# Kernel optimization log

Measured on AMD Instinct MI355X. Metric: run time of the kernel, lower is better.

Reference implementation:

```python
import jax, jax.numpy as jnp
import numpy as np

N = 200_000   # nodes in batched graph
E = 400_000   # edges
D = 128       # embed_dim
L = 5         # num_layer
G = 1000      # number of graphs in batch
ATOM_V = 119  # atom vocab (OGB)
BOND_V = 5    # bond vocab (OGB)
OUT = 128     # output_dim
EPS = 1e-5


def setup_inputs() -> dict:
    key = jax.random.key(0)
    ks = jax.random.split(key, 16)
    inp = {
        "nfeat": jax.random.randint(ks[0], (N,), 0, ATOM_V),
        "efeat": jax.random.randint(ks[1], (E,), 0, BOND_V),
        "src": jax.random.randint(ks[2], (E,), 0, N),
        "dst": jax.random.randint(ks[3], (E,), 0, N),
        "node2graph": jnp.sort(jax.random.randint(ks[4], (N,), 0, G)),
        # learned parameters
        "atom_emb": jax.random.normal(ks[5], (ATOM_V, D), jnp.float32) * 0.02,
        "edge_emb": jax.random.normal(ks[6], (L, BOND_V, D), jnp.float32) * 0.02,
        "W": jax.random.normal(ks[7], (L, D, D), jnp.float32) * 0.02,
        "b": jnp.zeros((L, D), jnp.float32),
        "gamma": jnp.ones((L, D), jnp.float32),
        "beta": jnp.zeros((L, D), jnp.float32),
        "W1": jax.random.normal(ks[8], (D, D), jnp.float32) * 0.02,
        "b1": jnp.zeros((D,), jnp.float32),
        "W2": jax.random.normal(ks[9], (D, OUT), jnp.float32) * 0.02,
        "b2": jnp.zeros((OUT,), jnp.float32),
    }
    return inp


def reference(nfeat, efeat, src, dst, node2graph,
              atom_emb, edge_emb, W, b, gamma, beta, W1, b1, W2, b2):
    h = atom_emb[nfeat]                                  # [N, D]
    # in-degree + 1 (GCNConvLayer degree norm)
    deg = jax.ops.segment_sum(jnp.ones((E,), h.dtype), dst, num_segments=N) + 1.0
    for l in range(L):
        e = edge_emb[l][efeat]                           # [E, D] edge encoder
        m = h[src] + e                                   # u_add_e
        neigh = jax.ops.segment_sum(m, dst, num_segments=N)  # fn.sum -> 'neigh'
        h = ((h + neigh) / deg[:, None]) @ W[l] + b[l]   # project_node_feat
        # batch norm over nodes (training-mode batch stats), affine
        mu = jnp.mean(h, axis=0)
        var = jnp.var(h, axis=0)
        h = (h - mu) * jax.lax.rsqrt(var + EPS) * gamma[l] + beta[l]
        h = jax.nn.relu(h)                               # activation; dropout=eval
    # global mean pooling per graph
    cnt = jax.ops.segment_sum(jnp.ones((N,), h.dtype), node2graph, num_segments=G)
    g = jax.ops.segment_sum(h, node2graph, num_segments=G) / jnp.maximum(cnt, 1.0)[:, None]
    # predict MLP (dropout in eval mode = identity)
    out = jax.nn.relu(g @ W1 + b1) @ W2 + b2             # [G, OUT]
    return out
```

## Files before the change

### kernel.cpp

```cpp
#include <hip/hip_runtime.h>
#include <hip/hip_bf16.h>
#include <cstddef>

#define NN 200000
#define NE 400000
#define DD 128
#define NL 5
#define NG 1000
#define BOND_V 5
#define BM 32
#define NBLK (NN / BM)
#define CAPE 256
#define CHUNK 200
#define NB_SCAN 200
#define CH 1000
#define EPS 1e-5f
#define XS 136

typedef __bf16 bf16x8 __attribute__((ext_vector_type(8)));
typedef float floatx4 __attribute__((ext_vector_type(4)));

__device__ __forceinline__ unsigned short f2bf(float f) {
    unsigned int u = __float_as_uint(f);
    u = (u + 0x7fffu + ((u >> 16) & 1u)) >> 16;
    return (unsigned short)u;
}
__device__ __forceinline__ float bf2f(unsigned short s) {
    return __uint_as_float(((unsigned int)s) << 16);
}

__global__ void k_deg_int(const int* __restrict__ dst, int* __restrict__ cnt) {
    int e = blockIdx.x * blockDim.x + threadIdx.x;
    if (e < NE) atomicAdd(&cnt[dst[e]], 1);
}

__global__ void k_cnt(const int* __restrict__ n2g, float* __restrict__ gcnt) {
    int n = blockIdx.x * blockDim.x + threadIdx.x;
    if (n < NN) atomicAdd(&gcnt[n2g[n]], 1.0f);
}

__global__ void k_rdeg(const int* __restrict__ cnt, float* __restrict__ rdeg) {
    int n = blockIdx.x * blockDim.x + threadIdx.x;
    if (n < NN) rdeg[n] = 1.0f / (float)(cnt[n] + 1);
}

__global__ void k_scan1(const int* __restrict__ cnt, int* __restrict__ bsum) {
    __shared__ int sh[256];
    int b = blockIdx.x, t = threadIdx.x;
    int s = 0;
    if (t < CH / 4) {
        int base = b * CH + t * 4;
        s = cnt[base] + cnt[base + 1] + cnt[base + 2] + cnt[base + 3];
    }
    sh[t] = s;
    __syncthreads();
    if (t == 0) {
        int tot = 0;
        for (int i = 0; i < CH / 4; i++) tot += sh[i];
        bsum[b] = tot;
    }
}

__global__ void k_scan2(const int* __restrict__ bsum, int* __restrict__ bpre,
                        int* __restrict__ off) {
    if (threadIdx.x == 0) {
        int run = 0;
        for (int i = 0; i < NB_SCAN; i++) { bpre[i] = run; run += bsum[i]; }
        off[NN] = NE;
    }
}

__global__ void k_scan3(const int* __restrict__ cnt, const int* __restrict__ bpre,
                        int* __restrict__ off, int* __restrict__ cur) {
    __shared__ int sh[256];
    int b = blockIdx.x, t = threadIdx.x;
    int base = b * CH + t * 4;
    int c0 = 0, c1 = 0, c2 = 0, c3 = 0, s = 0;
    if (t < CH / 4) {
        c0 = cnt[base]; c1 = cnt[base + 1]; c2 = cnt[base + 2]; c3 = cnt[base + 3];
        s = c0 + c1 + c2 + c3;
    }
    sh[t] = s;
    __syncthreads();
    if (t == 0) {
        int run = bpre[b];
        for (int i = 0; i < CH / 4; i++) { int v = sh[i]; sh[i] = run; run += v; }
    }
    __syncthreads();
    if (t < CH / 4) {
        int run = sh[t];
        off[base] = run; cur[base] = run; run += c0;
        off[base + 1] = run; cur[base + 1] = run; run += c1;
        off[base + 2] = run; cur[base + 2] = run; run += c2;
        off[base + 3] = run; cur[base + 3] = run;
    }
}

__global__ void k_bucket(const int* __restrict__ src, const int* __restrict__ dst,
                         const int* __restrict__ efeat, int* __restrict__ cur,
                         int* __restrict__ esrc, int* __restrict__ eft) {
    int e = blockIdx.x * blockDim.x + threadIdx.x;
    if (e < NE) {
        int p = atomicAdd(&cur[dst[e]], 1);
        esrc[p] = src[e];
        eft[p] = efeat[e];
    }
}

__global__ void k_wsplit(const float* __restrict__ W, unsigned short* __restrict__ Wht,
                         unsigned short* __restrict__ Wlt) {
    int idx = blockIdx.x * 256 + threadIdx.x;
    if (idx >= NL * DD * DD) return;
    int l = idx / (DD * DD), rem = idx % (DD * DD);
    int k = rem / DD, n = rem % DD;
    float v = W[idx];
    unsigned short hb = f2bf(v);
    unsigned short lb = f2bf(v - bf2f(hb));
    size_t o = (size_t)l * DD * DD + (size_t)n * DD + k;
    Wht[o] = hb; Wlt[o] = lb;
}

__device__ __forceinline__ float4 bnrelu4(float4 x, float4 m, float4 r, float4 g, float4 b) {
    float4 o;
    o.x = fmaxf(0.f, (x.x - m.x) * r.x * g.x + b.x);
    o.y = fmaxf(0.f, (x.y - m.y) * r.y * g.y + b.y);
    o.z = fmaxf(0.f, (x.z - m.z) * r.z * g.z + b.z);
    o.w = fmaxf(0.f, (x.w - m.w) * r.w * g.w + b.w);
    return o;
}

__global__ __launch_bounds__(256)
void k_fused(const float* __restrict__ base, const int* __restrict__ nfeat, int first,
             const int* __restrict__ off, const int* __restrict__ esrc,
             const int* __restrict__ eft, const float* __restrict__ eemb,
             const float* __restrict__ rdeg,
             const float* __restrict__ mu, const float* __restrict__ rsig,
             const float* __restrict__ gamma, const float* __restrict__ beta,
             const unsigned short* __restrict__ Wht, const unsigned short* __restrict__ Wlt,
             const float* __restrict__ bias,
             float* __restrict__ C, float* __restrict__ part) {
    __shared__ unsigned short Xh[BM * XS];
    __shared__ unsigned short Xl[BM * XS];
    __shared__ float eS[BOND_V * DD];
    __shared__ float red[4 * DD];
    __shared__ int esL[CAPE], efL[CAPE];
    __shared__ int offL[BM + 1];

    int tid = threadIdx.x;
    int n0 = blockIdx.x * BM;
    if (tid < BOND_V * DD / 4)
        *(float4*)(eS + tid * 4) = *(const float4*)(eemb + tid * 4);
    if (tid <= BM) offL[tid] = off[n0 + tid];
    int e_beg = off[n0], e_end = off[n0 + BM];
    for (int e = e_beg + tid; e < e_end; e += 256) {
        int idx = e - e_beg;
        if (idx < CAPE) { esL[idx] = esrc[e]; efL[idx] = eft[e]; }
    }

    int lane32 = tid & 31, grp = tid >> 5;
    int c4 = lane32 << 2;
    float4 m4, r4, g4, b4;
    if (!first) {
        m4 = *(const float4*)(mu + c4);
        r4 = *(const float4*)(rsig + c4);
        g4 = *(const float4*)(gamma + c4);
        b4 = *(const float4*)(beta + c4);
    }
    __syncthreads();

    bool lds_ok = (e_end - e_beg) <= CAPE;

    for (int i = 0; i < 4; i++) {
        int r = grp * 4 + i;
        int n = n0 + r;
        int rown = first ? nfeat[n] : n;
        float4 acc = *(const float4*)(base + (size_t)rown * DD + c4);
        if (!first) acc = bnrelu4(acc, m4, r4, g4, b4);
        int e0 = offL[r], e1 = offL[r + 1];
        int k = e0;
        if (lds_ok) {
            for (; k + 1 < e1; k += 2) {
                int i0 = k - e_beg;
                int s0 = esL[i0], f0 = efL[i0];
                int s1 = esL[i0 + 1], f1 = efL[i0 + 1];
                if (first) { s0 = nfeat[s0]; s1 = nfeat[s1]; }
                float4 h0 = *(const float4*)(base + (size_t)s0 * DD + c4);
                float4 h1 = *(const float4*)(base + (size_t)s1 * DD + c4);
                if (!first) { h0 = bnrelu4(h0, m4, r4, g4, b4); h1 = bnrelu4(h1, m4, r4, g4, b4); }
                float4 ev0 = *(const float4*)(eS + f0 * DD + c4);
                float4 ev1 = *(const float4*)(eS + f1 * DD + c4);
                acc.x += h0.x + ev0.x + h1.x + ev1.x;
                acc.y += h0.y + ev0.y + h1.y + ev1.y;
                acc.z += h0.z + ev0.z + h1.z + ev1.z;
                acc.w += h0.w + ev0.w + h1.w + ev1.w;
            }
            if (k < e1) {
                int i0 = k - e_beg;
                int s0 = esL[i0], f0 = efL[i0];
                if (first) s0 = nfeat[s0];
                float4 h0 = *(const float4*)(base + (size_t)s0 * DD + c4);
                if (!first) h0 = bnrelu4(h0, m4, r4, g4, b4);
                float4 ev0 = *(const float4*)(eS + f0 * DD + c4);
                acc.x += h0.x + ev0.x; acc.y += h0.y + ev0.y;
                acc.z += h0.z + ev0.z; acc.w += h0.w + ev0.w;
            }
        } else {
            for (; k < e1; k++) {
                int s0 = esrc[k], f0 = eft[k];
                if (first) s0 = nfeat[s0];
                float4 h0 = *(const float4*)(base + (size_t)s0 * DD + c4);
                if (!first) h0 = bnrelu4(h0, m4, r4, g4, b4);
                float4 ev0 = *(const float4*)(eS + f0 * DD + c4);
                acc.x += h0.x + ev0.x; acc.y += h0.y + ev0.y;
                acc.z += h0.z + ev0.z; acc.w += h0.w + ev0.w;
            }
        }
        float rd = rdeg[n];
        acc.x *= rd; acc.y *= rd; acc.z *= rd; acc.w *= rd;
        unsigned short h0 = f2bf(acc.x), h1 = f2bf(acc.y), h2 = f2bf(acc.z), h3 = f2bf(acc.w);
        unsigned short l0 = f2bf(acc.x - bf2f(h0));
        unsigned short l1 = f2bf(acc.y - bf2f(h1));
        unsigned short l2 = f2bf(acc.z - bf2f(h2));
        unsigned short l3 = f2bf(acc.w - bf2f(h3));
        uint2 hv2, lv2;
        hv2.x = (unsigned)h0 | ((unsigned)h1 << 16);
        hv2.y = (unsigned)h2 | ((unsigned)h3 << 16);
        lv2.x = (unsigned)l0 | ((unsigned)l1 << 16);
        lv2.y = (unsigned)l2 | ((unsigned)l3 << 16);
        *(uint2*)(Xh + r * XS + c4) = hv2;
        *(uint2*)(Xl + r * XS + c4) = lv2;
    }
    __syncthreads();

    int lane = tid & 63, w = tid >> 6;
    int m16 = lane & 15, quad = lane >> 4;
    int rowTile = w & 1;
    int colBase = (w >> 1) << 6;
    int rowA = rowTile * 16 + m16;

    floatx4 acc4[4];
    #pragma unroll
    for (int t = 0; t < 4; t++) acc4[t] = (floatx4){0.f, 0.f, 0.f, 0.f};

    #pragma unroll
    for (int kp = 0; kp < 4; kp++) {
        bf16x8 ah = *(const bf16x8*)(Xh + rowA * XS + kp * 32 + quad * 8);
        bf16x8 al = *(const bf16x8*)(Xl + rowA * XS + kp * 32 + quad * 8);
        #pragma unroll
        for (int t = 0; t < 4; t++) {
            int ncol = colBase + t * 16 + m16;
            bf16x8 bh = *(const bf16x8*)(Wht + (size_t)ncol * DD + kp * 32 + quad * 8);
            bf16x8 bl = *(const bf16x8*)(Wlt + (size_t)ncol * DD + kp * 32 + quad * 8);
            acc4[t] = __builtin_amdgcn_mfma_f32_16x16x32_bf16(ah, bh, acc4[t], 0, 0, 0);
            acc4[t] = __builtin_amdgcn_mfma_f32_16x16x32_bf16(ah, bl, acc4[t], 0, 0, 0);
            acc4[t] = __builtin_amdgcn_mfma_f32_16x16x32_bf16(al, bh, acc4[t], 0, 0, 0);
        }
    }

    float* redS = red;
    float* redQ = red + 2 * DD;
    #pragma unroll
    for (int t = 0; t < 4; t++) {
        int col = colBase + t * 16 + m16;
        float bv = bias[col];
        float s = 0.f, q = 0.f;
        #pragma unroll
        for (int rr = 0; rr < 4; rr++) {
            float v = acc4[t][rr] + bv;
            C[(size_t)(n0 + rowTile * 16 + quad * 4 + rr) * DD + col] = v;
            s += v; q += v * v;
        }
        s += __shfl_xor(s, 16); q += __shfl_xor(q, 16);
        s += __shfl_xor(s, 32); q += __shfl_xor(q, 32);
        if (lane < 16) { redS[rowTile * DD + col] = s; redQ[rowTile * DD + col] = q; }
    }
    __syncthreads();
    if (tid < DD) {
        float ss = redS[tid] + redS[DD + tid];
        float qq = redQ[tid] + redQ[DD + tid];
        part[(size_t)tid * NBLK + blockIdx.x] = ss;
        part[(size_t)(DD + tid) * NBLK + blockIdx.x] = qq;
    }
}

__global__ void k_stats(const float* __restrict__ part,
                        float* __restrict__ mu, float* __restrict__ rsig) {
    int col = blockIdx.x;
    float s = 0.f, q = 0.f;
    for (int i = threadIdx.x; i < NBLK; i += 256) {
        s += part[(size_t)col * NBLK + i];
        q += part[(size_t)(DD + col) * NBLK + i];
    }
    #pragma unroll
    for (int o = 32; o > 0; o >>= 1) {
        s += __shfl_down(s, o);
        q += __shfl_down(q, o);
    }
    __shared__ float sh[8];
    int lane = threadIdx.x & 63, w = threadIdx.x >> 6;
    if (lane == 0) { sh[w] = s; sh[4 + w] = q; }
    __syncthreads();
    if (threadIdx.x == 0) {
        float S = sh[0] + sh[1] + sh[2] + sh[3];
        float Q = sh[4] + sh[5] + sh[6] + sh[7];
        float m = S / (float)NN;
        float v = Q / (float)NN - m * m;
        mu[col] = m;
        rsig[col] = rsqrtf(v + EPS);
    }
}

__global__ void k_bnpool(const float* __restrict__ A, const int* __restrict__ n2g,
                         const float* __restrict__ mu, const float* __restrict__ rsig,
                         const float* __restrict__ gamma, const float* __restrict__ beta,
                         float* __restrict__ gsum) {
    int j = threadIdx.x;
    int n0 = blockIdx.x * CHUNK;
    float m = mu[j], r = rsig[j], ga = gamma[j], be = beta[j];
    int cur = n2g[n0];
    float acc = 0.f;
    for (int i = 0; i < CHUNK; i++) {
        int n = n0 + i;
        int gg = n2g[n];
        if (gg != cur) {
            atomicAdd(&gsum[(size_t)cur * DD + j], acc);
            acc = 0.f;
            cur = gg;
        }
        float x = A[(size_t)n * DD + j];
        x = fmaxf(0.f, (x - m) * r * ga + be);
        acc += x;
    }
    atomicAdd(&gsum[(size_t)cur * DD + j], acc);
}

__global__ void k_mlp(const float* __restrict__ gsum, const float* __restrict__ gcnt,
                      const float* __restrict__ W1, const float* __restrict__ b1,
                      const float* __restrict__ W2, const float* __restrict__ b2,
                      float* __restrict__ out) {
    __shared__ float gs[DD], hs[DD];
    int gid = blockIdx.x, j = threadIdx.x;
    float inv = 1.0f / fmaxf(gcnt[gid], 1.0f);
    gs[j] = gsum[(size_t)gid * DD + j] * inv;
    __syncthreads();
    float a = b1[j];
    for (int k = 0; k < DD; k++) a += gs[k] * W1[k * DD + j];
    hs[j] = fmaxf(a, 0.f);
    __syncthreads();
    float o = b2[j];
    for (int k = 0; k < DD; k++) o += hs[k] * W2[k * DD + j];
    out[(size_t)gid * DD + j] = o;
}

extern "C" void kernel_launch(void* const* d_in, const int* in_sizes, int n_in,
                              void* d_out, int out_size, void* d_ws, size_t ws_size,
                              hipStream_t stream) {
    const int*   nfeat = (const int*)d_in[0];
    const int*   efeat = (const int*)d_in[1];
    const int*   src   = (const int*)d_in[2];
    const int*   dst   = (const int*)d_in[3];
    const int*   n2g   = (const int*)d_in[4];
    const float* aemb  = (const float*)d_in[5];
    const float* eemb  = (const float*)d_in[6];
    const float* Wl    = (const float*)d_in[7];
    const float* bl    = (const float*)d_in[8];
    const float* gam   = (const float*)d_in[9];
    const float* bet   = (const float*)d_in[10];
    const float* W1    = (const float*)d_in[11];
    const float* b1    = (const float*)d_in[12];
    const float* W2    = (const float*)d_in[13];
    const float* b2    = (const float*)d_in[14];
    float* out = (float*)d_out;

    float* ws   = (float*)d_ws;
    float* H0   = ws;
    float* H1   = H0 + (size_t)NN * DD;
    float* rdeg = H1 + (size_t)NN * DD;
    float* gsum = rdeg + NN;
    float* gcnt = gsum + (size_t)NG * DD;
    float* mu   = gcnt + NG;
    float* rsg  = mu + DD;
    float* part = rsg + DD;
    unsigned short* Wht = (unsigned short*)(part + (size_t)2 * DD * NBLK);
    unsigned short* Wlt = Wht + (size_t)NL * DD * DD;
    int* off  = (int*)(Wlt + (size_t)NL * DD * DD);
    int* cur  = off + NN + 1;
    int* esrc = cur + NN;
    int* eft  = esrc + NE;
    int* cnt  = (int*)part;
    int* bsum = (int*)part + 300000;
    int* bpre = (int*)part + 301000;

    hipMemsetAsync(cnt, 0, (size_t)NN * sizeof(int), stream);
    hipMemsetAsync(gsum, 0, (size_t)(NG * DD + NG) * sizeof(float), stream);

    k_deg_int<<<(NE + 255) / 256, 256, 0, stream>>>(dst, cnt);
    k_cnt<<<(NN + 255) / 256, 256, 0, stream>>>(n2g, gcnt);
    k_scan1<<<NB_SCAN, 256, 0, stream>>>(cnt, bsum);
    k_scan2<<<1, 64, 0, stream>>>(bsum, bpre, off);
    k_scan3<<<NB_SCAN, 256, 0, stream>>>(cnt, bpre, off, cur);
    k_rdeg<<<(NN + 255) / 256, 256, 0, stream>>>(cnt, rdeg);
    k_bucket<<<(NE + 255) / 256, 256, 0, stream>>>(src, dst, efeat, cur, esrc, eft);
    k_wsplit<<<(NL * DD * DD + 255) / 256, 256, 0, stream>>>(Wl, Wht, Wlt);

    float* hcur = H0;
    for (int l = 0; l < NL; l++) {
        const float* base = (l == 0) ? aemb : hcur;
        float* hnext = (l == 0) ? H0 : ((hcur == H0) ? H1 : H0);
        const float* g_prev = (l == 0) ? gam : gam + (size_t)(l - 1) * DD;
        const float* b_prev = (l == 0) ? bet : bet + (size_t)(l - 1) * DD;
        k_fused<<<NBLK, 256, 0, stream>>>(base, nfeat, (l == 0) ? 1 : 0,
                                          off, esrc, eft,
                                          eemb + (size_t)l * BOND_V * DD, rdeg,
                                          mu, rsg, g_prev, b_prev,
                                          Wht + (size_t)l * DD * DD,
                                          Wlt + (size_t)l * DD * DD,
                                          bl + (size_t)l * DD, hnext, part);
        k_stats<<<DD, 256, 0, stream>>>(part, mu, rsg);
        hcur = hnext;
    }
    k_bnpool<<<NN / CHUNK, DD, 0, stream>>>(hcur, n2g, mu, rsg,
                                            gam + (size_t)(NL - 1) * DD,
                                            bet + (size_t)(NL - 1) * DD, gsum);
    k_mlp<<<NG, DD, 0, stream>>>(gsum, gcnt, W1, b1, W2, b2, out);
}
```

Before: 1.143 ms.

## Fuse setup kernels, edge-parallel LDS atomics, and last-block BN stats reduction

Merges the degree count, graph count and weight split into one setup kernel, and folds the reciprocal-degree computation into the scan. The per-node edge loop in the fused layer kernel becomes an edge-parallel loop. It accumulates into an fp32 LDS tile with shared-memory atomics, using the destination row packed into the edge feature word. The separate BN stats kernel is replaced by sharded global atomics with a last-block-done reduction inside the fused kernel. This removes launches and load imbalance between nodes of different degree, at the cost of LDS atomic contention and extra syncs.

```diff
diff --git a/kernel.cpp b/kernel.cpp
--- a/kernel.cpp
+++ b/kernel.cpp
@@ -16,6 +16,8 @@
 #define CH 1000
 #define EPS 1e-5f
 #define XS 136
+#define XFS 132
+#define NSH 32
 
 typedef __bf16 bf16x8 __attribute__((ext_vector_type(8)));
 typedef float floatx4 __attribute__((ext_vector_type(4)));
@@ -29,19 +31,22 @@
     return __uint_as_float(((unsigned int)s) << 16);
 }
 
-__global__ void k_deg_int(const int* __restrict__ dst, int* __restrict__ cnt) {
+__global__ void k_setup1(const int* __restrict__ dst, int* __restrict__ cnt,
+                         const int* __restrict__ n2g, float* __restrict__ gcnt,
+                         const float* __restrict__ W, unsigned short* __restrict__ Wht,
+                         unsigned short* __restrict__ Wlt) {
     int e = blockIdx.x * blockDim.x + threadIdx.x;
     if (e < NE) atomicAdd(&cnt[dst[e]], 1);
-}
-
-__global__ void k_cnt(const int* __restrict__ n2g, float* __restrict__ gcnt) {
-    int n = blockIdx.x * blockDim.x + threadIdx.x;
-    if (n < NN) atomicAdd(&gcnt[n2g[n]], 1.0f);
-}
-
-__global__ void k_rdeg(const int* __restrict__ cnt, float* __restrict__ rdeg) {
-    int n = blockIdx.x * blockDim.x + threadIdx.x;
-    if (n < NN) rdeg[n] = 1.0f / (float)(cnt[n] + 1);
+    if (e < NN) atomicAdd(&gcnt[n2g[e]], 1.0f);
+    if (e < NL * DD * DD) {
+        int l = e / (DD * DD), rem = e % (DD * DD);
+        int k = rem / DD, n = rem % DD;
+        float v = W[e];
+        unsigned short hb = f2bf(v);
+        unsigned short lb = f2bf(v - bf2f(hb));
+        size_t o = (size_t)l * DD * DD + (size_t)n * DD + k;
+        Wht[o] = hb; Wlt[o] = lb;
+    }
 }
 
 __global__ void k_scan1(const int* __restrict__ cnt, int* __restrict__ bsum) {
@@ -71,7 +76,8 @@
 }
 
 __global__ void k_scan3(const int* __restrict__ cnt, const int* __restrict__ bpre,
-                        int* __restrict__ off, int* __restrict__ cur) {
+                        int* __restrict__ off, int* __restrict__ cur,
+                        float* __restrict__ rdeg) {
     __shared__ int sh[256];
     int b = blockIdx.x, t = threadIdx.x;
     int base = b * CH + t * 4;
@@ -93,31 +99,23 @@
         off[base + 1] = run; cur[base + 1] = run; run += c1;
         off[base + 2] = run; cur[base + 2] = run; run += c2;
         off[base + 3] = run; cur[base + 3] = run;
+        rdeg[base]     = 1.0f / (float)(c0 + 1);
+        rdeg[base + 1] = 1.0f / (float)(c1 + 1);
+        rdeg[base + 2] = 1.0f / (float)(c2 + 1);
+        rdeg[base + 3] = 1.0f / (float)(c3 + 1);
     }
 }
 
 __global__ void k_bucket(const int* __restrict__ src, const int* __restrict__ dst,
                          const int* __restrict__ efeat, int* __restrict__ cur,
-                         int* __restrict__ esrc, int* __restrict__ eft) {
+                         int* __restrict__ esrc, int* __restrict__ epk) {
     int e = blockIdx.x * blockDim.x + threadIdx.x;
     if (e < NE) {
-        int p = atomicAdd(&cur[dst[e]], 1);
+        int d = dst[e];
+        int p = atomicAdd(&cur[d], 1);
         esrc[p] = src[e];
-        eft[p] = efeat[e];
-    }
-}
-
-__global__ void k_wsplit(const float* __restrict__ W, unsigned short* __restrict__ Wht,
-                         unsigned short* __restrict__ Wlt) {
-    int idx = blockIdx.x * 256 + threadIdx.x;
-    if (idx >= NL * DD * DD) return;
-    int l = idx / (DD * DD), rem = idx % (DD * DD);
-    int k = rem / DD, n = rem % DD;
-    float v = W[idx];
-    unsigned short hb = f2bf(v);
-    unsigned short lb = f2bf(v - bf2f(hb));
-    size_t o = (size_t)l * DD * DD + (size_t)n * DD + k;
-    Wht[o] = hb; Wlt[o] = lb;
+        epk[p] = efeat[e] | ((d & (BM - 1)) << 8);
+    }
 }
 
 __device__ __forceinline__ float4 bnrelu4(float4 x, float4 m, float4 r, float4 g, float4 b) {
@@ -132,96 +130,103 @@
 __global__ __launch_bounds__(256)
 void k_fused(const float* __restrict__ base, const int* __restrict__ nfeat, int first,
              const int* __restrict__ off, const int* __restrict__ esrc,
-             const int* __restrict__ eft, const float* __restrict__ eemb,
+             const int* __restrict__ epk, const float* __restrict__ eemb,
              const float* __restrict__ rdeg,
-             const float* __restrict__ mu, const float* __restrict__ rsig,
+             const float* __restrict__ muP, const float* __restrict__ rsP,
              const float* __restrict__ gamma, const float* __restrict__ beta,
              const unsigned short* __restrict__ Wht, const unsigned short* __restrict__ Wlt,
              const float* __restrict__ bias,
-             float* __restrict__ C, float* __restrict__ part) {
-    __shared__ unsigned short Xh[BM * XS];
-    __shared__ unsigned short Xl[BM * XS];
+             float* __restrict__ C,
+             float* __restrict__ musum, float* __restrict__ varsum,
+             int* __restrict__ cntL, float* __restrict__ muO, float* __restrict__ rsO) {
+    __shared__ float4 uni4[1088];
+    float* Xf = (float*)uni4;
+    unsigned short* Xh = (unsigned short*)uni4;
+    unsigned short* Xl = Xh + 4352;
     __shared__ float eS[BOND_V * DD];
     __shared__ float red[4 * DD];
-    __shared__ int esL[CAPE], efL[CAPE];
-    __shared__ int offL[BM + 1];
+    __shared__ int esL[CAPE], epkL[CAPE];
+    __shared__ int lastFlag;
 
     int tid = threadIdx.x;
     int n0 = blockIdx.x * BM;
     if (tid < BOND_V * DD / 4)
         *(float4*)(eS + tid * 4) = *(const float4*)(eemb + tid * 4);
-    if (tid <= BM) offL[tid] = off[n0 + tid];
     int e_beg = off[n0], e_end = off[n0 + BM];
+    int nE = e_end - e_beg;
     for (int e = e_beg + tid; e < e_end; e += 256) {
         int idx = e - e_beg;
-        if (idx < CAPE) { esL[idx] = esrc[e]; efL[idx] = eft[e]; }
+        if (idx < CAPE) { esL[idx] = esrc[e]; epkL[idx] = epk[e]; }
     }
 
     int lane32 = tid & 31, grp = tid >> 5;
     int c4 = lane32 << 2;
     float4 m4, r4, g4, b4;
     if (!first) {
-        m4 = *(const float4*)(mu + c4);
-        r4 = *(const float4*)(rsig + c4);
+        m4 = *(const float4*)(muP + c4);
+        r4 = *(const float4*)(rsP + c4);
         g4 = *(const float4*)(gamma + c4);
         b4 = *(const float4*)(beta + c4);
     }
-    __syncthreads();
-
-    bool lds_ok = (e_end - e_beg) <= CAPE;
-
+
+    #pragma unroll
     for (int i = 0; i < 4; i++) {
         int r = grp * 4 + i;
         int n = n0 + r;
         int rown = first ? nfeat[n] : n;
         float4 acc = *(const float4*)(base + (size_t)rown * DD + c4);
         if (!first) acc = bnrelu4(acc, m4, r4, g4, b4);
-        int e0 = offL[r], e1 = offL[r + 1];
-        int k = e0;
-        if (lds_ok) {
-            for (; k + 1 < e1; k += 2) {
-                int i0 = k - e_beg;
-                int s0 = esL[i0], f0 = efL[i0];
-                int s1 = esL[i0 + 1], f1 = efL[i0 + 1];
-                if (first) { s0 = nfeat[s0]; s1 = nfeat[s1]; }
-                float4 h0 = *(const float4*)(base + (size_t)s0 * DD + c4);
-                float4 h1 = *(const float4*)(base + (size_t)s1 * DD + c4);
-                if (!first) { h0 = bnrelu4(h0, m4, r4, g4, b4); h1 = bnrelu4(h1, m4, r4, g4, b4); }
-                float4 ev0 = *(const float4*)(eS + f0 * DD + c4);
-                float4 ev1 = *(const float4*)(eS + f1 * DD + c4);
-                acc.x += h0.x + ev0.x + h1.x + ev1.x;
-                acc.y += h0.y + ev0.y + h1.y + ev1.y;
-                acc.z += h0.z + ev0.z + h1.z + ev1.z;
-                acc.w += h0.w + ev0.w + h1.w + ev1.w;
-            }
-            if (k < e1) {
-                int i0 = k - e_beg;
-                int s0 = esL[i0], f0 = efL[i0];
-                if (first) s0 = nfeat[s0];
-                float4 h0 = *(const float4*)(base + (size_t)s0 * DD + c4);
-                if (!first) h0 = bnrelu4(h0, m4, r4, g4, b4);
-                float4 ev0 = *(const float4*)(eS + f0 * DD + c4);
-                acc.x += h0.x + ev0.x; acc.y += h0.y + ev0.y;
-                acc.z += h0.z + ev0.z; acc.w += h0.w + ev0.w;
-            }
-        } else {
-            for (; k < e1; k++) {
-                int s0 = esrc[k], f0 = eft[k];
-                if (first) s0 = nfeat[s0];
-                float4 h0 = *(const float4*)(base + (size_t)s0 * DD + c4);
-                if (!first) h0 = bnrelu4(h0, m4, r4, g4, b4);
-                float4 ev0 = *(const float4*)(eS + f0 * DD + c4);
-                acc.x += h0.x + ev0.x; acc.y += h0.y + ev0.y;
-                acc.z += h0.z + ev0.z; acc.w += h0.w + ev0.w;
-            }
-        }
-        float rd = rdeg[n];
-        acc.x *= rd; acc.y *= rd; acc.z *= rd; acc.w *= rd;
-        unsigned short h0 = f2bf(acc.x), h1 = f2bf(acc.y), h2 = f2bf(acc.z), h3 = f2bf(acc.w);
-        unsigned short l0 = f2bf(acc.x - bf2f(h0));
-        unsigned short l1 = f2bf(acc.y - bf2f(h1));
-        unsigned short l2 = f2bf(acc.z - bf2f(h2));
-        unsigned short l3 = f2bf(acc.w - bf2f(h3));
+        *(float4*)(Xf + r * XFS + c4) = acc;
+    }
+    __syncthreads();
+
+    if (nE <= CAPE) {
+        for (int k = grp; k < nE; k += 8) {
+            int s = esL[k], pk = epkL[k];
+            if (first) s = nfeat[s];
+            float4 hv = *(const float4*)(base + (size_t)s * DD + c4);
+            if (!first) hv = bnrelu4(hv, m4, r4, g4, b4);
+            const float* ep = eS + (pk & 255) * DD + c4;
+            float* xp = Xf + (pk >> 8) * XFS + c4;
+            atomicAdd(xp + 0, hv.x + ep[0]);
+            atomicAdd(xp + 1, hv.y + ep[1]);
+            atomicAdd(xp + 2, hv.z + ep[2]);
+            atomicAdd(xp + 3, hv.w + ep[3]);
+        }
+    } else {
+        for (int k = e_beg + grp; k < e_end; k += 8) {
+            int s = esrc[k], pk = epk[k];
+            if (first) s = nfeat[s];
+            float4 hv = *(const float4*)(base + (size_t)s * DD + c4);
+            if (!first) hv = bnrelu4(hv, m4, r4, g4, b4);
+            const float* ep = eS + (pk & 255) * DD + c4;
+            float* xp = Xf + (pk >> 8) * XFS + c4;
+            atomicAdd(xp + 0, hv.x + ep[0]);
+            atomicAdd(xp + 1, hv.y + ep[1]);
+            atomicAdd(xp + 2, hv.z + ep[2]);
+            atomicAdd(xp + 3, hv.w + ep[3]);
+        }
+    }
+    __syncthreads();
+
+    float4 v[4];
+    #pragma unroll
+    for (int i = 0; i < 4; i++) {
+        int r = grp * 4 + i;
+        v[i] = *(const float4*)(Xf + r * XFS + c4);
+        float rd = rdeg[n0 + r];
+        v[i].x *= rd; v[i].y *= rd; v[i].z *= rd; v[i].w *= rd;
+    }
+    __syncthreads();
+
+    #pragma unroll
+    for (int i = 0; i < 4; i++) {
+        int r = grp * 4 + i;
+        unsigned short h0 = f2bf(v[i].x), h1 = f2bf(v[i].y), h2 = f2bf(v[i].z), h3 = f2bf(v[i].w);
+        unsigned short l0 = f2bf(v[i].x - bf2f(h0));
+        unsigned short l1 = f2bf(v[i].y - bf2f(h1));
+        unsigned short l2 = f2bf(v[i].z - bf2f(h2));
+        unsigned short l3 = f2bf(v[i].w - bf2f(h3));
         uint2 hv2, lv2;
         hv2.x = (unsigned)h0 | ((unsigned)h1 << 16);
         hv2.y = (unsigned)h2 | ((unsigned)h3 << 16);
@@ -266,47 +271,37 @@
         float s = 0.f, q = 0.f;
         #pragma unroll
         for (int rr = 0; rr < 4; rr++) {
-            float v = acc4[t][rr] + bv;
-            C[(size_t)(n0 + rowTile * 16 + quad * 4 + rr) * DD + col] = v;
-            s += v; q += v * v;
+            float vv = acc4[t][rr] + bv;
+            C[(size_t)(n0 + rowTile * 16 + quad * 4 + rr) * DD + col] = vv;
+            s += vv; q += vv * vv;
         }
         s += __shfl_xor(s, 16); q += __shfl_xor(q, 16);
         s += __shfl_xor(s, 32); q += __shfl_xor(q, 32);
         if (lane < 16) { redS[rowTile * DD + col] = s; redQ[rowTile * DD + col] = q; }
     }
     __syncthreads();
+    int shard = blockIdx.x & (NSH - 1);
     if (tid < DD) {
         float ss = redS[tid] + redS[DD + tid];
         float qq = redQ[tid] + redQ[DD + tid];
-        part[(size_t)tid * NBLK + blockIdx.x] = ss;
-        part[(size_t)(DD + tid) * NBLK + blockIdx.x] = qq;
-    }
-}
-
-__global__ void k_stats(const float* __restrict__ part,
-                        float* __restrict__ mu, float* __restrict__ rsig) {
-    int col = blockIdx.x;
-    float s = 0.f, q = 0.f;
-    for (int i = threadIdx.x; i < NBLK; i += 256) {
-        s += part[(size_t)col * NBLK + i];
-        q += part[(size_t)(DD + col) * NBLK + i];
-    }
-    #pragma unroll
-    for (int o = 32; o > 0; o >>= 1) {
-        s += __shfl_down(s, o);
-        q += __shfl_down(q, o);
-    }
-    __shared__ float sh[8];
-    int lane = threadIdx.x & 63, w = threadIdx.x >> 6;
-    if (lane == 0) { sh[w] = s; sh[4 + w] = q; }
-    __syncthreads();
-    if (threadIdx.x == 0) {
-        float S = sh[0] + sh[1] + sh[2] + sh[3];
-        float Q = sh[4] + sh[5] + sh[6] + sh[7];
+        atomicAdd(&musum[tid * NSH + shard], ss);
+        atomicAdd(&varsum[tid * NSH + shard], qq);
+        __threadfence();
+    }
+    __syncthreads();
+    if (tid == 0) lastFlag = (atomicAdd(cntL, 1) == NBLK - 1);
+    __syncthreads();
+    if (lastFlag && tid < DD) {
+        float S = 0.f, Q = 0.f;
+        #pragma unroll
+        for (int sh = 0; sh < NSH; sh++) {
+            S += atomicAdd(&musum[tid * NSH + sh], 0.0f);
+            Q += atomicAdd(&varsum[tid * NSH + sh], 0.0f);
+        }
         float m = S / (float)NN;
-        float v = Q / (float)NN - m * m;
-        mu[col] = m;
-        rsig[col] = rsqrtf(v + EPS);
+        float va = Q / (float)NN - m * m;
+        muO[tid] = m;
+        rsO[tid] = rsqrtf(va + EPS);
     }
 }
 
@@ -372,54 +367,62 @@
     const float* b2    = (const float*)d_in[14];
     float* out = (float*)d_out;
 
-    float* ws   = (float*)d_ws;
-    float* H0   = ws;
-    float* H1   = H0 + (size_t)NN * DD;
-    float* rdeg = H1 + (size_t)NN * DD;
-    float* gsum = rdeg + NN;
-    float* gcnt = gsum + (size_t)NG * DD;
-    float* mu   = gcnt + NG;
-    float* rsg  = mu + DD;
-    float* part = rsg + DD;
-    unsigned short* Wht = (unsigned short*)(part + (size_t)2 * DD * NBLK);
+    float* ws    = (float*)d_ws;
+    float* H0    = ws;
+    float* H1    = H0 + (size_t)NN * DD;
+    float* rdeg  = H1 + (size_t)NN * DD;
+    float* gsum  = rdeg + NN;
+    float* gcnt  = gsum + (size_t)NG * DD;
+    float* muA   = gcnt + NG;
+    float* rsA   = muA + NL * DD;
+    float* musum = rsA + NL * DD;
+    float* varsum= musum + (size_t)NL * DD * NSH;
+    int*   cntL  = (int*)(varsum + (size_t)NL * DD * NSH);
+    unsigned short* Wht = (unsigned short*)(cntL + 16);
     unsigned short* Wlt = Wht + (size_t)NL * DD * DD;
     int* off  = (int*)(Wlt + (size_t)NL * DD * DD);
     int* cur  = off + NN + 1;
     int* esrc = cur + NN;
-    int* eft  = esrc + NE;
-    int* cnt  = (int*)part;
-    int* bsum = (int*)part + 300000;
-    int* bpre = (int*)part + 301000;
-
+    int* epk  = esrc + NE;
+    int* cnt  = epk + NE;
+    int* bsum = cnt + NN;
+    int* bpre = bsum + NB_SCAN;
+
+    hipMemsetAsync(gsum, 0, (size_t)(NG * DD + NG) * sizeof(float), stream);
+    hipMemsetAsync(musum, 0, (size_t)(2 * NL * DD * NSH) * sizeof(float) + 16 * sizeof(int), stream);
     hipMemsetAsync(cnt, 0, (size_t)NN * sizeof(int), stream);
-    hipMemsetAsync(gsum, 0, (size_t)(NG * DD + NG) * sizeof(float), stream);
-
-    k_deg_int<<<(NE + 255) / 256, 256, 0, stream>>>(dst, cnt);
-    k_cnt<<<(NN + 255) / 256, 256, 0, stream>>>(n2g, gcnt);
+
+    k_setup1<<<(NE + 255) / 256, 256, 0, stream>>>(dst, cnt, n2g, gcnt, Wl, Wht, Wlt);
     k_scan1<<<NB_SCAN, 256, 0, stream>>>(cnt, bsum);
     k_scan2<<<1, 64, 0, stream>>>(bsum, bpre, off);
-    k_scan3<<<NB_SCAN, 256, 0, stream>>>(cnt, bpre, off, cur);
-    k_rdeg<<<(NN + 255) / 256, 256, 0, stream>>>(cnt, rdeg);
-    k_bucket<<<(NE + 255) / 256, 256, 0, stream>>>(src, dst, efeat, cur, esrc, eft);
-    k_wsplit<<<(NL * DD * DD + 255) / 256, 256, 0, stream>>>(Wl, Wht, Wlt);
+    k_scan3<<<NB_SCAN, 256, 0, stream>>>(cnt, bpre, off, cur, rdeg);
+    k_bucket<<<(NE + 255) / 256, 256, 0, stream>>>(src, dst, efeat, cur, esrc, epk);
 
     float* hcur = H0;
     for (int l = 0; l < NL; l++) {
         const float* base = (l == 0) ? aemb : hcur;
         float* hnext = (l == 0) ? H0 : ((hcur == H0) ? H1 : H0);
+        const float* muP = (l == 0) ? muA : muA + (size_t)(l - 1) * DD;
+        const float* rsP = (l == 0) ? rsA : rsA + (size_t)(l - 1) * DD;
         const float* g_prev = (l == 0) ? gam : gam + (size_t)(l - 1) * DD;
         const float* b_prev = (l == 0) ? bet : bet + (size_t)(l - 1) * DD;
         k_fused<<<NBLK, 256, 0, stream>>>(base, nfeat, (l == 0) ? 1 : 0,
-                                          off, esrc, eft,
+                                          off, esrc, epk,
                                           eemb + (size_t)l * BOND_V * DD, rdeg,
-                                          mu, rsg, g_prev, b_prev,
+                                          muP, rsP, g_prev, b_prev,
                                           Wht + (size_t)l * DD * DD,
                                           Wlt + (size_t)l * DD * DD,
-                                          bl + (size_t)l * DD, hnext, part);
-        k_stats<<<DD, 256, 0, stream>>>(part, mu, rsg);
+                                          bl + (size_t)l * DD, hnext,
+                                          musum + (size_t)l * DD * NSH,
+                                          varsum + (size_t)l * DD * NSH,
+                                          cntL + l,
+                                          muA + (size_t)l * DD,
+                                          rsA + (size_t)l * DD);
         hcur = hnext;
     }
-    k_bnpool<<<NN / CHUNK, DD, 0, stream>>>(hcur, n2g, mu, rsg,
+    k_bnpool<<<NN / CHUNK, DD, 0, stream>>>(hcur, n2g,
+                                            muA + (size_t)(NL - 1) * DD,
+                                            rsA + (size_t)(NL - 1) * DD,
                                             gam + (size_t)(NL - 1) * DD,
                                             bet + (size_t)(NL - 1) * DD, gsum);
     k_mlp<<<NG, DD, 0, stream>>>(gsum, gcnt, W1, b1, W2, b2, out);
```

Measured after the change: 3.401 ms. +197.5%, slower.

## Pad per-block edge lists into column-major packed layout for batched gathers

Applied to the files above, without the earlier changes.

Adds a preprocessing kernel that, for each 32-node block, packs each node's first 16 incoming edges (source index plus bond type in one int) into a padded column-major array, with a dummy bond type that maps to a zero row. The aggregation loop then processes four rows per step with independent gathers, which is meant to raise memory-level parallelism and remove the per-block LDS staging and its sync. Edges beyond 16 fall back to a scalar loop. Setup kernels are also merged (degree count, graph count and weight split in one launch; reciprocal degree folded into the scan), which trims launch overhead. The cost is wasted loads on padded slots when degrees within a block differ.

```diff
diff --git a/kernel.cpp b/kernel.cpp
--- a/kernel.cpp
+++ b/kernel.cpp
@@ -10,7 +10,7 @@
 #define BOND_V 5
 #define BM 32
 #define NBLK (NN / BM)
-#define CAPE 256
+#define MAXD 16
 #define CHUNK 200
 #define NB_SCAN 200
 #define CH 1000
@@ -29,19 +29,22 @@
     return __uint_as_float(((unsigned int)s) << 16);
 }
 
-__global__ void k_deg_int(const int* __restrict__ dst, int* __restrict__ cnt) {
+__global__ void k_setup1(const int* __restrict__ dst, int* __restrict__ cnt,
+                         const int* __restrict__ n2g, float* __restrict__ gcnt,
+                         const float* __restrict__ W, unsigned short* __restrict__ Wht,
+                         unsigned short* __restrict__ Wlt) {
     int e = blockIdx.x * blockDim.x + threadIdx.x;
     if (e < NE) atomicAdd(&cnt[dst[e]], 1);
-}
-
-__global__ void k_cnt(const int* __restrict__ n2g, float* __restrict__ gcnt) {
-    int n = blockIdx.x * blockDim.x + threadIdx.x;
-    if (n < NN) atomicAdd(&gcnt[n2g[n]], 1.0f);
-}
-
-__global__ void k_rdeg(const int* __restrict__ cnt, float* __restrict__ rdeg) {
-    int n = blockIdx.x * blockDim.x + threadIdx.x;
-    if (n < NN) rdeg[n] = 1.0f / (float)(cnt[n] + 1);
+    if (e < NN) atomicAdd(&gcnt[n2g[e]], 1.0f);
+    if (e < NL * DD * DD) {
+        int l = e / (DD * DD), rem = e % (DD * DD);
+        int k = rem / DD, n = rem % DD;
+        float v = W[e];
+        unsigned short hb = f2bf(v);
+        unsigned short lb = f2bf(v - bf2f(hb));
+        size_t o = (size_t)l * DD * DD + (size_t)n * DD + k;
+        Wht[o] = hb; Wlt[o] = lb;
+    }
 }
 
 __global__ void k_scan1(const int* __restrict__ cnt, int* __restrict__ bsum) {
@@ -71,7 +74,8 @@
 }
 
 __global__ void k_scan3(const int* __restrict__ cnt, const int* __restrict__ bpre,
-                        int* __restrict__ off, int* __restrict__ cur) {
+                        int* __restrict__ off, int* __restrict__ cur,
+                        float* __restrict__ rdeg) {
     __shared__ int sh[256];
     int b = blockIdx.x, t = threadIdx.x;
     int base = b * CH + t * 4;
@@ -93,6 +97,10 @@
         off[base + 1] = run; cur[base + 1] = run; run += c1;
         off[base + 2] = run; cur[base + 2] = run; run += c2;
         off[base + 3] = run; cur[base + 3] = run;
+        rdeg[base]     = 1.0f / (float)(c0 + 1);
+        rdeg[base + 1] = 1.0f / (float)(c1 + 1);
+        rdeg[base + 2] = 1.0f / (float)(c2 + 1);
+        rdeg[base + 3] = 1.0f / (float)(c3 + 1);
     }
 }
 
@@ -107,17 +115,30 @@
     }
 }
 
-__global__ void k_wsplit(const float* __restrict__ W, unsigned short* __restrict__ Wht,
-                         unsigned short* __restrict__ Wlt) {
-    int idx = blockIdx.x * 256 + threadIdx.x;
-    if (idx >= NL * DD * DD) return;
-    int l = idx / (DD * DD), rem = idx % (DD * DD);
-    int k = rem / DD, n = rem % DD;
-    float v = W[idx];
-    unsigned short hb = f2bf(v);
-    unsigned short lb = f2bf(v - bf2f(hb));
-    size_t o = (size_t)l * DD * DD + (size_t)n * DD + k;
-    Wht[o] = hb; Wlt[o] = lb;
+__global__ void k_pad(const int* __restrict__ off, const int* __restrict__ esrc,
+                      const int* __restrict__ eft, int* __restrict__ pent,
+                      int* __restrict__ bmaxd) {
+    __shared__ int offL[BM + 1];
+    __shared__ int mx;
+    int b = blockIdx.x, tid = threadIdx.x;
+    if (tid == 0) mx = 0;
+    if (tid <= BM) offL[tid] = off[b * BM + tid];
+    __syncthreads();
+    if (tid < BM) atomicMax(&mx, offL[tid + 1] - offL[tid]);
+    __syncthreads();
+    int maxd = mx;
+    if (tid == 0) bmaxd[b] = maxd;
+    int jmax = maxd < MAXD ? maxd : MAXD;
+    int tot = jmax * BM;
+    int* pb = pent + (size_t)b * MAXD * BM;
+    for (int idx = tid; idx < tot; idx += 256) {
+        int j = idx >> 5, r = idx & 31;
+        int d = offL[r + 1] - offL[r];
+        int v;
+        if (j < d) { int e = offL[r] + j; v = esrc[e] | (eft[e] << 18); }
+        else v = (5 << 18);
+        pb[idx] = v;
+    }
 }
 
 __device__ __forceinline__ float4 bnrelu4(float4 x, float4 m, float4 r, float4 g, float4 b) {
@@ -132,96 +153,114 @@
 __global__ __launch_bounds__(256)
 void k_fused(const float* __restrict__ base, const int* __restrict__ nfeat, int first,
              const int* __restrict__ off, const int* __restrict__ esrc,
-             const int* __restrict__ eft, const float* __restrict__ eemb,
+             const int* __restrict__ eft, const int* __restrict__ pent,
+             const int* __restrict__ bmaxd, const float* __restrict__ eemb,
              const float* __restrict__ rdeg,
-             const float* __restrict__ mu, const float* __restrict__ rsig,
+             const float* __restrict__ muP, const float* __restrict__ rsP,
              const float* __restrict__ gamma, const float* __restrict__ beta,
              const unsigned short* __restrict__ Wht, const unsigned short* __restrict__ Wlt,
              const float* __restrict__ bias,
              float* __restrict__ C, float* __restrict__ part) {
     __shared__ unsigned short Xh[BM * XS];
     __shared__ unsigned short Xl[BM * XS];
-    __shared__ float eS[BOND_V * DD];
+    __shared__ float eS[6 * DD];
     __shared__ float red[4 * DD];
-    __shared__ int esL[CAPE], efL[CAPE];
     __shared__ int offL[BM + 1];
 
     int tid = threadIdx.x;
     int n0 = blockIdx.x * BM;
-    if (tid < BOND_V * DD / 4)
-        *(float4*)(eS + tid * 4) = *(const float4*)(eemb + tid * 4);
+    if (tid < 160) *(float4*)(eS + tid * 4) = *(const float4*)(eemb + tid * 4);
+    else if (tid < 192) *(float4*)(eS + tid * 4) = (float4){0.f, 0.f, 0.f, 0.f};
     if (tid <= BM) offL[tid] = off[n0 + tid];
-    int e_beg = off[n0], e_end = off[n0 + BM];
-    for (int e = e_beg + tid; e < e_end; e += 256) {
-        int idx = e - e_beg;
-        if (idx < CAPE) { esL[idx] = esrc[e]; efL[idx] = eft[e]; }
-    }
 
     int lane32 = tid & 31, grp = tid >> 5;
     int c4 = lane32 << 2;
     float4 m4, r4, g4, b4;
     if (!first) {
-        m4 = *(const float4*)(mu + c4);
-        r4 = *(const float4*)(rsig + c4);
+        m4 = *(const float4*)(muP + c4);
+        r4 = *(const float4*)(rsP + c4);
         g4 = *(const float4*)(gamma + c4);
         b4 = *(const float4*)(beta + c4);
     }
     __syncthreads();
 
-    bool lds_ok = (e_end - e_beg) <= CAPE;
-
+    float4 acc[4];
+    #pragma unroll
+    for (int i = 0; i < 4; i++) {
+        int n = n0 + grp * 4 + i;
+        int rown = first ? nfeat[n] : n;
+        float4 a = *(const float4*)(base + (size_t)rown * DD + c4);
+        if (!first) a = bnrelu4(a, m4, r4, g4, b4);
+        acc[i] = a;
+    }
+
+    int maxd = bmaxd[blockIdx.x];
+    int jmax = maxd < MAXD ? maxd : MAXD;
+    const int* pb = pent + (size_t)blockIdx.x * MAXD * BM + grp * 4;
+    for (int j = 0; j < jmax; j++) {
+        int v0 = pb[j * BM + 0];
+        int v1 = pb[j * BM + 1];
+        int v2 = pb[j * BM + 2];
+        int v3 = pb[j * BM + 3];
+        int s0 = v0 & 0x3FFFF, f0 = v0 >> 18;
+        int s1 = v1 & 0x3FFFF, f1 = v1 >> 18;
+        int s2 = v2 & 0x3FFFF, f2 = v2 >> 18;
+        int s3 = v3 & 0x3FFFF, f3 = v3 >> 18;
+        if (first) { s0 = nfeat[s0]; s1 = nfeat[s1]; s2 = nfeat[s2]; s3 = nfeat[s3]; }
+        float4 h0 = *(const float4*)(base + (size_t)s0 * DD + c4);
+        float4 h1 = *(const float4*)(base + (size_t)s1 * DD + c4);
+        float4 h2 = *(const float4*)(base + (size_t)s2 * DD + c4);
+        float4 h3 = *(const float4*)(base + (size_t)s3 * DD + c4);
+        if (!first) {
+            h0 = bnrelu4(h0, m4, r4, g4, b4);
+            h1 = bnrelu4(h1, m4, r4, g4, b4);
+            h2 = bnrelu4(h2, m4, r4, g4, b4);
+            h3 = bnrelu4(h3, m4, r4, g4, b4);
+        }
+        float w0 = (f0 == 5) ? 0.f : 1.f;
+        float w1 = (f1 == 5) ? 0.f : 1.f;
+        float w2 = (f2 == 5) ? 0.f : 1.f;
+        float w3 = (f3 == 5) ? 0.f : 1.f;
+        float4 e0 = *(const float4*)(eS + f0 * DD + c4);
+        float4 e1 = *(const float4*)(eS + f1 * DD + c4);
+        float4 e2 = *(const float4*)(eS + f2 * DD + c4);
+        float4 e3 = *(const float4*)(eS + f3 * DD + c4);
+        acc[0].x += (h0.x + e0.x) * w0; acc[0].y += (h0.y + e0.y) * w0;
+        acc[0].z += (h0.z + e0.z) * w0; acc[0].w += (h0.w + e0.w) * w0;
+        acc[1].x += (h1.x + e1.x) * w1; acc[1].y += (h1.y + e1.y) * w1;
+        acc[1].z += (h1.z + e1.z) * w1; acc[1].w += (h1.w + e1.w) * w1;
+        acc[2].x += (h2.x + e2.x) * w2; acc[2].y += (h2.y + e2.y) * w2;
+        acc[2].z += (h2.z + e2.z) * w2; acc[2].w += (h2.w + e2.w) * w2;
+        acc[3].x += (h3.x + e3.x) * w3; acc[3].y += (h3.y + e3.y) * w3;
+        acc[3].z += (h3.z + e3.z) * w3; acc[3].w += (h3.w + e3.w) * w3;
+    }
+
+    if (maxd > MAXD) {
+        #pragma unroll
+        for (int i = 0; i < 4; i++) {
+            int r = grp * 4 + i;
+            for (int e = offL[r] + MAXD; e < offL[r + 1]; e++) {
+                int s = esrc[e], f = eft[e];
+                if (first) s = nfeat[s];
+                float4 hv = *(const float4*)(base + (size_t)s * DD + c4);
+                if (!first) hv = bnrelu4(hv, m4, r4, g4, b4);
+                const float* ep = eS + f * DD + c4;
+                acc[i].x += hv.x + ep[0]; acc[i].y += hv.y + ep[1];
+                acc[i].z += hv.z + ep[2]; acc[i].w += hv.w + ep[3];
+            }
+        }
+    }
+
+    #pragma unroll
     for (int i = 0; i < 4; i++) {
         int r = grp * 4 + i;
-        int n = n0 + r;
-        int rown = first ? nfeat[n] : n;
-        float4 acc = *(const float4*)(base + (size_t)rown * DD + c4);
-        if (!first) acc = bnrelu4(acc, m4, r4, g4, b4);
-        int e0 = offL[r], e1 = offL[r + 1];
-        int k = e0;
-        if (lds_ok) {
-            for (; k + 1 < e1; k += 2) {
-                int i0 = k - e_beg;
-                int s0 = esL[i0], f0 = efL[i0];
-                int s1 = esL[i0 + 1], f1 = efL[i0 + 1];
-                if (first) { s0 = nfeat[s0]; s1 = nfeat[s1]; }
-                float4 h0 = *(const float4*)(base + (size_t)s0 * DD + c4);
-                float4 h1 = *(const float4*)(base + (size_t)s1 * DD + c4);
-                if (!first) { h0 = bnrelu4(h0, m4, r4, g4, b4); h1 = bnrelu4(h1, m4, r4, g4, b4); }
-                float4 ev0 = *(const float4*)(eS + f0 * DD + c4);
-                float4 ev1 = *(const float4*)(eS + f1 * DD + c4);
-                acc.x += h0.x + ev0.x + h1.x + ev1.x;
-                acc.y += h0.y + ev0.y + h1.y + ev1.y;
-                acc.z += h0.z + ev0.z + h1.z + ev1.z;
-                acc.w += h0.w + ev0.w + h1.w + ev1.w;
-            }
-            if (k < e1) {
-                int i0 = k - e_beg;
-                int s0 = esL[i0], f0 = efL[i0];
-                if (first) s0 = nfeat[s0];
-                float4 h0 = *(const float4*)(base + (size_t)s0 * DD + c4);
-                if (!first) h0 = bnrelu4(h0, m4, r4, g4, b4);
-                float4 ev0 = *(const float4*)(eS + f0 * DD + c4);
-                acc.x += h0.x + ev0.x; acc.y += h0.y + ev0.y;
-                acc.z += h0.z + ev0.z; acc.w += h0.w + ev0.w;
-            }
-        } else {
-            for (; k < e1; k++) {
-                int s0 = esrc[k], f0 = eft[k];
-                if (first) s0 = nfeat[s0];
-                float4 h0 = *(const float4*)(base + (size_t)s0 * DD + c4);
-                if (!first) h0 = bnrelu4(h0, m4, r4, g4, b4);
-                float4 ev0 = *(const float4*)(eS + f0 * DD + c4);
-                acc.x += h0.x + ev0.x; acc.y += h0.y + ev0.y;
-                acc.z += h0.z + ev0.z; acc.w += h0.w + ev0.w;
-            }
-        }
-        float rd = rdeg[n];
-        acc.x *= rd; acc.y *= rd; acc.z *= rd; acc.w *= rd;
-        unsigned short h0 = f2bf(acc.x), h1 = f2bf(acc.y), h2 = f2bf(acc.z), h3 = f2bf(acc.w);
-        unsigned short l0 = f2bf(acc.x - bf2f(h0));
-        unsigned short l1 = f2bf(acc.y - bf2f(h1));
-        unsigned short l2 = f2bf(acc.z - bf2f(h2));
-        unsigned short l3 = f2bf(acc.w - bf2f(h3));
+        float rd = rdeg[n0 + r];
+        float ax = acc[i].x * rd, ay = acc[i].y * rd, az = acc[i].z * rd, aw = acc[i].w * rd;
+        unsigned short h0 = f2bf(ax), h1 = f2bf(ay), h2 = f2bf(az), h3 = f2bf(aw);
+        unsigned short l0 = f2bf(ax - bf2f(h0));
+        unsigned short l1 = f2bf(ay - bf2f(h1));
+        unsigned short l2 = f2bf(az - bf2f(h2));
+        unsigned short l3 = f2bf(aw - bf2f(h3));
         uint2 hv2, lv2;
         hv2.x = (unsigned)h0 | ((unsigned)h1 << 16);
         hv2.y = (unsigned)h2 | ((unsigned)h3 << 16);
@@ -266,9 +305,9 @@
         float s = 0.f, q = 0.f;
         #pragma unroll
         for (int rr = 0; rr < 4; rr++) {
-            float v = acc4[t][rr] + bv;
-            C[(size_t)(n0 + rowTile * 16 + quad * 4 + rr) * DD + col] = v;
-            s += v; q += v * v;
+            float vv = acc4[t][rr] + bv;
+            C[(size_t)(n0 + rowTile * 16 + quad * 4 + rr) * DD + col] = vv;
+            s += vv; q += vv * vv;
         }
         s += __shfl_xor(s, 16); q += __shfl_xor(q, 16);
         s += __shfl_xor(s, 32); q += __shfl_xor(q, 32);
@@ -383,25 +422,25 @@
     float* part = rsg + DD;
     unsigned short* Wht = (unsigned short*)(part + (size_t)2 * DD * NBLK);
     unsigned short* Wlt = Wht + (size_t)NL * DD * DD;
-    int* off  = (int*)(Wlt + (size_t)NL * DD * DD);
-    int* cur  = off + NN + 1;
-    int* esrc = cur + NN;
-    int* eft  = esrc + NE;
-    int* cnt  = (int*)part;
-    int* bsum = (int*)part + 300000;
-    int* bpre = (int*)part + 301000;
-
+    int* off   = (int*)(Wlt + (size_t)NL * DD * DD);
+    int* cur   = off + NN + 1;
+    int* esrc  = cur + NN;
+    int* eft   = esrc + NE;
+    int* cnt   = eft + NE;
+    int* bsum  = cnt + NN;
+    int* bpre  = bsum + NB_SCAN;
+    int* bmaxd = bpre + NB_SCAN;
+    int* pent  = bmaxd + NBLK;
+
+    hipMemsetAsync(gsum, 0, (size_t)(NG * DD + NG) * sizeof(float), stream);
     hipMemsetAsync(cnt, 0, (size_t)NN * sizeof(int), stream);
-    hipMemsetAsync(gsum, 0, (size_t)(NG * DD + NG) * sizeof(float), stream);
-
-    k_deg_int<<<(NE + 255) / 256, 256, 0, stream>>>(dst, cnt);
-    k_cnt<<<(NN + 255) / 256, 256, 0, stream>>>(n2g, gcnt);
+
+    k_setup1<<<(NE + 255) / 256, 256, 0, stream>>>(dst, cnt, n2g, gcnt, Wl, Wht, Wlt);
     k_scan1<<<NB_SCAN, 256, 0, stream>>>(cnt, bsum);
     k_scan2<<<1, 64, 0, stream>>>(bsum, bpre, off);
-    k_scan3<<<NB_SCAN, 256, 0, stream>>>(cnt, bpre, off, cur);
-    k_rdeg<<<(NN + 255) / 256, 256, 0, stream>>>(cnt, rdeg);
+    k_scan3<<<NB_SCAN, 256, 0, stream>>>(cnt, bpre, off, cur, rdeg);
     k_bucket<<<(NE + 255) / 256, 256, 0, stream>>>(src, dst, efeat, cur, esrc, eft);
-    k_wsplit<<<(NL * DD * DD + 255) / 256, 256, 0, stream>>>(Wl, Wht, Wlt);
+    k_pad<<<NBLK, 256, 0, stream>>>(off, esrc, eft, pent, bmaxd);
 
     float* hcur = H0;
     for (int l = 0; l < NL; l++) {
@@ -410,7 +449,7 @@
         const float* g_prev = (l == 0) ? gam : gam + (size_t)(l - 1) * DD;
         const float* b_prev = (l == 0) ? bet : bet + (size_t)(l - 1) * DD;
         k_fused<<<NBLK, 256, 0, stream>>>(base, nfeat, (l == 0) ? 1 : 0,
-                                          off, esrc, eft,
+                                          off, esrc, eft, pent, bmaxd,
                                           eemb + (size_t)l * BOND_V * DD, rdeg,
                                           mu, rsg, g_prev, b_prev,
                                           Wht + (size_t)l * DD * DD,
```

Result: no change. 1.163 ms (+1.7%).
